# Optimization experiments

Measured on AMD Instinct MI355X. Metric: run time of the kernel, lower is better.

The kernel has to match this reference:

```python
import jax, jax.numpy as jnp
import numpy as np

NUM_FEATURES = 256   # 2**8
BOND_DIM = 16
N_CORES = 8          # log2(NUM_FEATURES)
BATCH = 262144


def _mpo_cores(mpo_weights, n, bond_dim):
    # Slice the flat parameter vector into n cores of shape (l, r, 2, 2).
    shapes = [(1, bond_dim, 2, 2)] + [(bond_dim, bond_dim, 2, 2)] * (n - 2) + [(bond_dim, 1, 2, 2)]
    cores, off = [], 0
    for s in shapes:
        sz = int(np.prod(s))
        cores.append(mpo_weights[off:off + sz].reshape(s))
        off += sz
    return cores


def _contract_mpo(cores):
    # Sequentially contract the tensor-train cores into the full (2^n, 2^n) matrix.
    # T has axes (bond, I, J) where I/J accumulate the row/col physical bits
    # in order i1..in / j1..jn, matching the original einsum + reshape.
    T = cores[0][0]          # (r, 2, 2)
    dim = 2
    for A in cores[1:]:      # A: (l, r2, 2, 2)
        T = jnp.einsum('aIJ,abkm->bIkJm', T, A).reshape(A.shape[1], dim * 2, dim * 2)
        dim *= 2
    return T[0]              # (2^n, 2^n)


def setup_inputs() -> dict:
    key = jax.random.key(0)
    k1, k2, k3 = jax.random.split(key, 3)
    total = 2 * 4 * BOND_DIM + (N_CORES - 2) * 4 * BOND_DIM ** 2  # 6272
    return {
        'x': jax.random.normal(k1, (BATCH, NUM_FEATURES), dtype=jnp.float32),
        'mpo_weights': jax.random.normal(k2, (total,), dtype=jnp.float32) * 0.1,
        'dense_kernel': jax.random.normal(k3, (NUM_FEATURES, 1), dtype=jnp.float32) * 0.1,
        'dense_bias': jnp.zeros((1,), dtype=jnp.float32),
    }


def reference(x, mpo_weights, dense_kernel, dense_bias):
    W = _contract_mpo(_mpo_cores(mpo_weights, N_CORES, BOND_DIM))  # (256, 256)
    h = jnp.square(x @ W)                                          # (B, 256)
    return h @ dense_kernel + dense_bias                           # (B, 1)
```

## Files before the change

kernel.cpp:

```cpp
#include <hip/hip_runtime.h>
#include <hip/hip_bf16.h>

typedef _Float16 half8 __attribute__((ext_vector_type(8)));
typedef float    floatx4 __attribute__((ext_vector_type(4)));

#define WSCALE      4096.0f
#define WSCALE_INV  (1.0f/(4096.0f*4096.0f))

#define WF16_OFF 8192

__global__ __launch_bounds__(256)
void mpo_prep(const float* __restrict__ w, _Float16* __restrict__ Wf) {
    __shared__ __align__(16) float wL[6272];
    __shared__ __align__(16) float sL[8704];
    __shared__ __align__(16) float tuL[8192];
    const int tid = threadIdx.x;

    {
        const floatx4* s4 = reinterpret_cast<const floatx4*>(w);
        floatx4* d4 = reinterpret_cast<floatx4*>(wL);
        for (int i = tid; i < 1568; i += 256) d4[i] = s4[i];
    }
    __syncthreads();

    {
        int li = tid;
        int mm = li & 3, kk = (li >> 2) & 3, c = li >> 4;
        int k1 = kk >> 1, k2 = kk & 1, m1 = mm >> 1, m2 = mm & 1;
        float s = 0.f;
#pragma unroll
        for (int b = 0; b < 16; ++b)
            s += wL[b * 4 + k1 * 2 + m1] * wL[64 + b * 64 + c * 4 + k2 * 2 + m2];
        sL[li] = s;
    }
    {
        const int i0 = (tid >> 4) * 4, j0 = (tid & 15) * 4;
        const float* Ab = wL + 1088 + (i0 >> 2) * 64;
        const float* Bb = wL + 2112 + j0;
        float acc[4][4] = {};
#pragma unroll
        for (int b = 0; b < 16; ++b) {
            floatx4 ar = *reinterpret_cast<const floatx4*>(Ab + b * 4);
            floatx4 br = *reinterpret_cast<const floatx4*>(Bb + b * 64);
#pragma unroll
            for (int r = 0; r < 4; ++r)
#pragma unroll
                for (int s = 0; s < 4; ++s) acc[r][s] += ar[r] * br[s];
        }
#pragma unroll
        for (int r = 0; r < 4; ++r)
#pragma unroll
        for (int s = 0; s < 4; ++s) {
            int i = i0 + r, j = j0 + s;
            sL[256 + (i >> 2) * 256 + (j >> 2) * 16 +
               ((i >> 1) & 1) * 8 + ((j >> 1) & 1) * 4 + (i & 1) * 2 + (j & 1)] = acc[r][s];
        }
    }
    {
        const int i0 = (tid >> 4) * 4, j0 = (tid & 15) * 4;
        const float* Ab = wL + 3136 + (i0 >> 2) * 64;
        const float* Bb = wL + 4160 + j0;
        float acc[4][4] = {};
#pragma unroll
        for (int b = 0; b < 16; ++b) {
            floatx4 ar = *reinterpret_cast<const floatx4*>(Ab + b * 4);
            floatx4 br = *reinterpret_cast<const floatx4*>(Bb + b * 64);
#pragma unroll
            for (int r = 0; r < 4; ++r)
#pragma unroll
                for (int s = 0; s < 4; ++s) acc[r][s] += ar[r] * br[s];
        }
#pragma unroll
        for (int r = 0; r < 4; ++r)
#pragma unroll
        for (int s = 0; s < 4; ++s) {
            int i = i0 + r, j = j0 + s;
            sL[4352 + (i >> 2) * 256 + (j >> 2) * 16 +
               ((i >> 1) & 1) * 8 + ((j >> 1) & 1) * 4 + (i & 1) * 2 + (j & 1)] = acc[r][s];
        }
    }
    {
        int li = tid;
        int mm = li & 3, kk = (li >> 2) & 3, a = li >> 4;
        int k1 = kk >> 1, k2 = kk & 1, m1 = mm >> 1, m2 = mm & 1;
        float s = 0.f;
#pragma unroll
        for (int b = 0; b < 16; ++b)
            s += wL[5184 + a * 64 + b * 4 + k1 * 2 + m1] * wL[6208 + b * 4 + k2 * 2 + m2];
        sL[8448 + li] = s;
    }
    __syncthreads();

    {
        const int p0 = (tid >> 6) * 4, q0 = (tid & 63) * 4;
        float acc[4][4] = {};
#pragma unroll
        for (int a = 0; a < 16; ++a) {
            floatx4 pr = *reinterpret_cast<const floatx4*>(sL + a * 16 + p0);
            floatx4 qr = *reinterpret_cast<const floatx4*>(sL + 256 + a * 256 + q0);
#pragma unroll
            for (int r = 0; r < 4; ++r)
#pragma unroll
                for (int s = 0; s < 4; ++s) acc[r][s] += pr[r] * qr[s];
        }
#pragma unroll
        for (int r = 0; r < 4; ++r)
#pragma unroll
        for (int s = 0; s < 4; ++s) {
            int p = p0 + r, q = q0 + s;
            tuL[(q >> 4) * 256 + ((p >> 2) * 4 + ((q >> 2) & 3)) * 16 +
                (p & 3) * 4 + (q & 3)] = acc[r][s];
        }
    }
    {
        const int r0 = (tid >> 2) * 4, q0 = (tid & 3) * 4;
        float acc[4][4] = {};
#pragma unroll
        for (int b = 0; b < 16; ++b) {
            floatx4 ar = *reinterpret_cast<const floatx4*>(sL + 4352 + (r0 >> 4) * 256 + b * 16 + (r0 & 15));
            floatx4 br = *reinterpret_cast<const floatx4*>(sL + 8448 + b * 16 + q0);
#pragma unroll
            for (int r = 0; r < 4; ++r)
#pragma unroll
                for (int s = 0; s < 4; ++s) acc[r][s] += ar[r] * br[s];
        }
#pragma unroll
        for (int r = 0; r < 4; ++r)
#pragma unroll
        for (int s = 0; s < 4; ++s)
            tuL[4096 + (r0 + r) * 16 + q0 + s] = acc[r][s];
    }
    __syncthreads();

    {
        int idx = blockIdx.x * 256 + tid;
        int J4 = idx & 255, I4 = idx >> 8;
        int I16 = I4 >> 4, kc = (I4 >> 2) & 3, k2v = I4 & 3;
        int mc = (J4 >> 2) & 3, m2v = J4 & 3;
        int J16 = J4 >> 4;
        const float* Uc = tuL + 4096 + (((kc * 4 + mc) * 4 + k2v) * 4 + m2v);
        float s = 0.f;
#pragma unroll
        for (int a = 0; a < 16; ++a)
            s += tuL[(a * 16 + I16) * 16 + J16] * Uc[a * 256];
        int nn = J4 >> 4, lr = J4 & 15, kq = I4 >> 5, gg = (I4 >> 3) & 3, jj = I4 & 7;
        Wf[(((nn * 8 + kq) * 64) + gg * 16 + lr) * 8 + jj] = (_Float16)(s * WSCALE);
    }
}

__global__ __launch_bounds__(512, 2)
void mpo_main(const float* __restrict__ x, const _Float16* __restrict__ Wf,
              const float* __restrict__ dk, const float* __restrict__ bias,
              float* __restrict__ out) {
    extern __shared__ _Float16 Wl[];
    float* dkL = reinterpret_cast<float*>(Wl + 65536);

    const int tid  = threadIdx.x;
    const int lane = tid & 63;
    const int wave = tid >> 6;
    const int lrow = lane & 15;
    const int g    = lane >> 4;

    const long blockbase = (long)blockIdx.x * 1024;
    const float* xb = x + (blockbase + wave * 16 + lrow) * 256 + g * 8;
    const int SET_STRIDE = 128 * 256;

    half8 a[8];
    floatx4 lo[8], hi[8];

#define SB()  __builtin_amdgcn_sched_barrier(0)
#define XLD(i, xn) do { const float* p_ = (xn) + (i) * 32;              \
                     lo[i] = *reinterpret_cast<const floatx4*>(p_);     \
                     hi[i] = *reinterpret_cast<const floatx4*>(p_ + 4); } while (0)
#define XLD_ALL(xn) do { XLD(0,xn); XLD(1,xn); XLD(2,xn); XLD(3,xn); \
                         XLD(4,xn); XLD(5,xn); XLD(6,xn); XLD(7,xn); } while (0)
#define XCVT(i) do { half8 f_;                                                \
                     f_[0] = (_Float16)lo[i][0]; f_[1] = (_Float16)lo[i][1];  \
                     f_[2] = (_Float16)lo[i][2]; f_[3] = (_Float16)lo[i][3];  \
                     f_[4] = (_Float16)hi[i][0]; f_[5] = (_Float16)hi[i][1];  \
                     f_[6] = (_Float16)hi[i][2]; f_[7] = (_Float16)hi[i][3];  \
                     a[i] = f_; } while (0)
#define XCVT_ALL() do { XCVT(0); XCVT(1); XCVT(2); XCVT(3); \
                        XCVT(4); XCVT(5); XCVT(6); XCVT(7); } while (0)

    XLD_ALL(xb);
    SB();
    {
        const floatx4* src = reinterpret_cast<const floatx4*>(Wf);
        floatx4* dst = reinterpret_cast<floatx4*>(Wl);
#pragma unroll
        for (int i = 0; i < 16; ++i)
            dst[tid + i * 512] = src[tid + i * 512];
    }
    if (tid < 256) dkL[tid] = dk[tid];
    const float bs = bias[0];
    __syncthreads();

    float kreg[16];
#pragma unroll
    for (int n = 0; n < 16; ++n) kreg[n] = dkL[n * 16 + lrow];

    XCVT_ALL();
    XLD_ALL(xb + SET_STRIDE);
    SB();

    const half8* Wv = reinterpret_cast<const half8*>(Wl);

#pragma unroll 1
    for (int s = 0; s < 8; ++s) {
        float rp[4] = {0, 0, 0, 0};
#pragma unroll 1
        for (int n = 0; n < 16; ++n) {
            const half8* Wn = Wv + n * 512 + lane;
            floatx4 c0 = {0, 0, 0, 0};
#pragma unroll
            for (int kk = 0; kk < 8; ++kk)
                c0 = __builtin_amdgcn_mfma_f32_16x16x32_f16(a[kk], Wn[kk * 64], c0, 0, 0, 0);
            const float kv = kreg[n];
#pragma unroll
            for (int r = 0; r < 4; ++r)
                rp[r] += c0[r] * c0[r] * kv;
        }

        if (s < 7) { XCVT_ALL(); }
        if (s < 6) { XLD_ALL(xb + (s + 2) * SET_STRIDE); }
        SB();

#pragma unroll
        for (int r = 0; r < 4; ++r) {
            float v = rp[r];
            v += __shfl_xor(v, 1);
            v += __shfl_xor(v, 2);
            v += __shfl_xor(v, 4);
            v += __shfl_xor(v, 8);
            rp[r] = v;
        }
        if (lrow == 0) {
            floatx4 o;
#pragma unroll
            for (int r = 0; r < 4; ++r) o[r] = rp[r] * WSCALE_INV + bs;
            *reinterpret_cast<floatx4*>(out + blockbase + s * 128 + wave * 16 + g * 4) = o;
        }
        SB();
    }
}

extern "C" void kernel_launch(void* const* d_in, const int* in_sizes, int n_in,
                              void* d_out, int out_size, void* d_ws, size_t ws_size,
                              hipStream_t stream) {
    const float* x    = (const float*)d_in[0];
    const float* w    = (const float*)d_in[1];
    const float* dk   = (const float*)d_in[2];
    const float* bias = (const float*)d_in[3];
    float* out = (float*)d_out;
    float* ws  = (float*)d_ws;

    _Float16* Wf16 = (_Float16*)(ws + WF16_OFF);

    static bool attr_set = false;
    if (!attr_set) {
        hipFuncSetAttribute((const void*)mpo_main,
                            hipFuncAttributeMaxDynamicSharedMemorySize, 132096);
        attr_set = true;
    }

    mpo_prep<<<256, 256, 0, stream>>>(w, Wf16);

    mpo_main<<<256, 512, 132096, stream>>>(x, Wf16, dk, bias, out);
}
```

Before: 62.60 us.

## Process two row tiles per wave to reuse each LDS weight fragment twice

Each wave now handles two 16-row tiles at once, so every W fragment loaded from LDS feeds two MFMAs and LDS read traffic per row is halved. The loop runs 4 passes of 256 rows instead of 8 of 128, with double x prefetch buffers (A and B sets). kreg is dropped in favour of reading dk from LDS inside the loop, which frees registers for the extra buffers. The cost is much higher VGPR pressure under launch_bounds(512,2), which may cause spills or lower occupancy, and fewer passes leave less room for the prefetch to overlap with compute.

Measured after the change: 92.11 us. 47.1% more time.

```diff
diff --git a/kernel.cpp b/kernel.cpp
--- a/kernel.cpp
+++ b/kernel.cpp
@@ -162,28 +162,32 @@
     const int g    = lane >> 4;
 
     const long blockbase = (long)blockIdx.x * 1024;
-    const float* xb = x + (blockbase + wave * 16 + lrow) * 256 + g * 8;
-    const int SET_STRIDE = 128 * 256;
-
-    half8 a[8];
-    floatx4 lo[8], hi[8];
+    const float* xb = x + (blockbase + wave * 32 + lrow) * 256 + g * 8;
+    const int PASS_STRIDE = 256 * 256;
+    const int SET_STRIDE  = 16 * 256;
+
+    half8 a0[8], a1[8];
+    floatx4 loA[8], hiA[8], loB[8], hiB[8];
 
 #define SB()  __builtin_amdgcn_sched_barrier(0)
-#define XLD(i, xn) do { const float* p_ = (xn) + (i) * 32;              \
-                     lo[i] = *reinterpret_cast<const floatx4*>(p_);     \
-                     hi[i] = *reinterpret_cast<const floatx4*>(p_ + 4); } while (0)
-#define XLD_ALL(xn) do { XLD(0,xn); XLD(1,xn); XLD(2,xn); XLD(3,xn); \
-                         XLD(4,xn); XLD(5,xn); XLD(6,xn); XLD(7,xn); } while (0)
-#define XCVT(i) do { half8 f_;                                                \
-                     f_[0] = (_Float16)lo[i][0]; f_[1] = (_Float16)lo[i][1];  \
-                     f_[2] = (_Float16)lo[i][2]; f_[3] = (_Float16)lo[i][3];  \
-                     f_[4] = (_Float16)hi[i][0]; f_[5] = (_Float16)hi[i][1];  \
-                     f_[6] = (_Float16)hi[i][2]; f_[7] = (_Float16)hi[i][3];  \
-                     a[i] = f_; } while (0)
-#define XCVT_ALL() do { XCVT(0); XCVT(1); XCVT(2); XCVT(3); \
-                        XCVT(4); XCVT(5); XCVT(6); XCVT(7); } while (0)
-
-    XLD_ALL(xb);
+#define XLD8(lo, hi, xn) do { _Pragma("unroll")                          \
+    for (int i_ = 0; i_ < 8; ++i_) {                                     \
+        const float* p_ = (xn) + i_ * 32;                                \
+        lo[i_] = *reinterpret_cast<const floatx4*>(p_);                  \
+        hi[i_] = *reinterpret_cast<const floatx4*>(p_ + 4);              \
+    } } while (0)
+#define XCVT8(a, lo, hi) do { _Pragma("unroll")                          \
+    for (int i_ = 0; i_ < 8; ++i_) {                                     \
+        half8 f_;                                                        \
+        f_[0] = (_Float16)lo[i_][0]; f_[1] = (_Float16)lo[i_][1];        \
+        f_[2] = (_Float16)lo[i_][2]; f_[3] = (_Float16)lo[i_][3];        \
+        f_[4] = (_Float16)hi[i_][0]; f_[5] = (_Float16)hi[i_][1];        \
+        f_[6] = (_Float16)hi[i_][2]; f_[7] = (_Float16)hi[i_][3];        \
+        a[i_] = f_;                                                      \
+    } } while (0)
+
+    XLD8(loA, hiA, xb);
+    XLD8(loB, hiB, xb + SET_STRIDE);
     SB();
     {
         const floatx4* src = reinterpret_cast<const floatx4*>(Wf);
@@ -196,50 +200,61 @@
     const float bs = bias[0];
     __syncthreads();
 
-    float kreg[16];
-#pragma unroll
-    for (int n = 0; n < 16; ++n) kreg[n] = dkL[n * 16 + lrow];
-
-    XCVT_ALL();
-    XLD_ALL(xb + SET_STRIDE);
+    XCVT8(a0, loA, hiA);
+    XLD8(loA, hiA, xb + PASS_STRIDE);
+    XCVT8(a1, loB, hiB);
+    XLD8(loB, hiB, xb + PASS_STRIDE + SET_STRIDE);
     SB();
 
     const half8* Wv = reinterpret_cast<const half8*>(Wl);
 
 #pragma unroll 1
-    for (int s = 0; s < 8; ++s) {
-        float rp[4] = {0, 0, 0, 0};
+    for (int p = 0; p < 4; ++p) {
+        float rp0[4] = {0, 0, 0, 0}, rp1[4] = {0, 0, 0, 0};
 #pragma unroll 1
         for (int n = 0; n < 16; ++n) {
+            const float kv = dkL[n * 16 + lrow];
             const half8* Wn = Wv + n * 512 + lane;
-            floatx4 c0 = {0, 0, 0, 0};
-#pragma unroll
-            for (int kk = 0; kk < 8; ++kk)
-                c0 = __builtin_amdgcn_mfma_f32_16x16x32_f16(a[kk], Wn[kk * 64], c0, 0, 0, 0);
-            const float kv = kreg[n];
-#pragma unroll
-            for (int r = 0; r < 4; ++r)
-                rp[r] += c0[r] * c0[r] * kv;
-        }
-
-        if (s < 7) { XCVT_ALL(); }
-        if (s < 6) { XLD_ALL(xb + (s + 2) * SET_STRIDE); }
-        SB();
+            floatx4 c0 = {0, 0, 0, 0}, c1 = {0, 0, 0, 0};
+#pragma unroll
+            for (int kk = 0; kk < 8; ++kk) {
+                half8 b = Wn[kk * 64];
+                c0 = __builtin_amdgcn_mfma_f32_16x16x32_f16(a0[kk], b, c0, 0, 0, 0);
+                c1 = __builtin_amdgcn_mfma_f32_16x16x32_f16(a1[kk], b, c1, 0, 0, 0);
+            }
+#pragma unroll
+            for (int r = 0; r < 4; ++r) {
+                rp0[r] += c0[r] * c0[r] * kv;
+                rp1[r] += c1[r] * c1[r] * kv;
+            }
+        }
 
 #pragma unroll
         for (int r = 0; r < 4; ++r) {
-            float v = rp[r];
-            v += __shfl_xor(v, 1);
-            v += __shfl_xor(v, 2);
-            v += __shfl_xor(v, 4);
-            v += __shfl_xor(v, 8);
-            rp[r] = v;
+            float v0 = rp0[r], v1 = rp1[r];
+            v0 += __shfl_xor(v0, 1); v1 += __shfl_xor(v1, 1);
+            v0 += __shfl_xor(v0, 2); v1 += __shfl_xor(v1, 2);
+            v0 += __shfl_xor(v0, 4); v1 += __shfl_xor(v1, 4);
+            v0 += __shfl_xor(v0, 8); v1 += __shfl_xor(v1, 8);
+            rp0[r] = v0; rp1[r] = v1;
         }
         if (lrow == 0) {
-            floatx4 o;
-#pragma unroll
-            for (int r = 0; r < 4; ++r) o[r] = rp[r] * WSCALE_INV + bs;
-            *reinterpret_cast<floatx4*>(out + blockbase + s * 128 + wave * 16 + g * 4) = o;
+            floatx4 o0, o1;
+#pragma unroll
+            for (int r = 0; r < 4; ++r) {
+                o0[r] = rp0[r] * WSCALE_INV + bs;
+                o1[r] = rp1[r] * WSCALE_INV + bs;
+            }
+            float* ob = out + blockbase + p * 256 + wave * 32 + g * 4;
+            *reinterpret_cast<floatx4*>(ob)      = o0;
+            *reinterpret_cast<floatx4*>(ob + 16) = o1;
+        }
+
+        if (p < 3) {
+            XCVT8(a0, loA, hiA);
+            if (p < 2) { XLD8(loA, hiA, xb + (p + 2) * PASS_STRIDE); }
+            XCVT8(a1, loB, hiB);
+            if (p < 2) { XLD8(loB, hiB, xb + (p + 2) * PASS_STRIDE + SET_STRIDE); }
         }
         SB();
     }
```

## Switch main GEMM to 32x32x16 MFMA tiles with half-split x pipelining

Applied to the files above, without the earlier changes.

Replaces the 16x16x32 MFMA tiling with 32x32x16 MFMA, so each wave processes 32 rows per step and the precomputed W is stored in a matching layout. x loads are split into two halves double-buffered across iterations, and the reduction and output stores are reworked for the 32-wide accumulator. This cuts LDS reads of W per FLOP and the number of MFMA issues, at the cost of more accumulator registers (16 floats for c and 16 for rp), which may lower occupancy or cause spills.

Measured after the change: 66.34 us. +6.0%, slower.

```diff
diff --git a/kernel.cpp b/kernel.cpp
--- a/kernel.cpp
+++ b/kernel.cpp
@@ -3,6 +3,7 @@
 
 typedef _Float16 half8 __attribute__((ext_vector_type(8)));
 typedef float    floatx4 __attribute__((ext_vector_type(4)));
+typedef float    floatx16 __attribute__((ext_vector_type(16)));
 
 #define WSCALE      4096.0f
 #define WSCALE_INV  (1.0f/(4096.0f*4096.0f))
@@ -143,8 +144,8 @@
 #pragma unroll
         for (int a = 0; a < 16; ++a)
             s += tuL[(a * 16 + I16) * 16 + J16] * Uc[a * 256];
-        int nn = J4 >> 4, lr = J4 & 15, kq = I4 >> 5, gg = (I4 >> 3) & 3, jj = I4 & 7;
-        Wf[(((nn * 8 + kq) * 64) + gg * 16 + lr) * 8 + jj] = (_Float16)(s * WSCALE);
+        int nn = J4 >> 5, cc = J4 & 31, kq = I4 >> 4, hh = (I4 >> 3) & 1, jj = I4 & 7;
+        Wf[(((nn * 16 + kq) * 64) + hh * 32 + cc) * 8 + jj] = (_Float16)(s * WSCALE);
     }
 }
 
@@ -158,32 +159,34 @@
     const int tid  = threadIdx.x;
     const int lane = tid & 63;
     const int wave = tid >> 6;
-    const int lrow = lane & 15;
-    const int g    = lane >> 4;
+    const int col  = lane & 31;
+    const int hi   = lane >> 5;
 
     const long blockbase = (long)blockIdx.x * 1024;
-    const float* xb = x + (blockbase + wave * 16 + lrow) * 256 + g * 8;
-    const int SET_STRIDE = 128 * 256;
-
-    half8 a[8];
-    floatx4 lo[8], hi[8];
+    const float* xr = x + (blockbase + wave * 32 + col) * 256 + hi * 8;
+    const int SS = 256 * 256;
+
+    half8 a[16];
+    floatx4 lob[8], hib[8];
 
 #define SB()  __builtin_amdgcn_sched_barrier(0)
-#define XLD(i, xn) do { const float* p_ = (xn) + (i) * 32;              \
-                     lo[i] = *reinterpret_cast<const floatx4*>(p_);     \
-                     hi[i] = *reinterpret_cast<const floatx4*>(p_ + 4); } while (0)
-#define XLD_ALL(xn) do { XLD(0,xn); XLD(1,xn); XLD(2,xn); XLD(3,xn); \
-                         XLD(4,xn); XLD(5,xn); XLD(6,xn); XLD(7,xn); } while (0)
-#define XCVT(i) do { half8 f_;                                                \
-                     f_[0] = (_Float16)lo[i][0]; f_[1] = (_Float16)lo[i][1];  \
-                     f_[2] = (_Float16)lo[i][2]; f_[3] = (_Float16)lo[i][3];  \
-                     f_[4] = (_Float16)hi[i][0]; f_[5] = (_Float16)hi[i][1];  \
-                     f_[6] = (_Float16)hi[i][2]; f_[7] = (_Float16)hi[i][3];  \
-                     a[i] = f_; } while (0)
-#define XCVT_ALL() do { XCVT(0); XCVT(1); XCVT(2); XCVT(3); \
-                        XCVT(4); XCVT(5); XCVT(6); XCVT(7); } while (0)
-
-    XLD_ALL(xb);
+#define XLDH(s, h) do { _Pragma("unroll")                                \
+    for (int i_ = 0; i_ < 8; ++i_) {                                     \
+        const float* p_ = xr + (s) * SS + ((h) * 8 + i_) * 16;           \
+        lob[i_] = *reinterpret_cast<const floatx4*>(p_);                 \
+        hib[i_] = *reinterpret_cast<const floatx4*>(p_ + 4);             \
+    } } while (0)
+#define XCVTH(h) do { _Pragma("unroll")                                  \
+    for (int i_ = 0; i_ < 8; ++i_) {                                     \
+        half8 f_;                                                        \
+        f_[0] = (_Float16)lob[i_][0]; f_[1] = (_Float16)lob[i_][1];      \
+        f_[2] = (_Float16)lob[i_][2]; f_[3] = (_Float16)lob[i_][3];      \
+        f_[4] = (_Float16)hib[i_][0]; f_[5] = (_Float16)hib[i_][1];      \
+        f_[6] = (_Float16)hib[i_][2]; f_[7] = (_Float16)hib[i_][3];      \
+        a[(h) * 8 + i_] = f_;                                            \
+    } } while (0)
+
+    XLDH(0, 0);
     SB();
     {
         const floatx4* src = reinterpret_cast<const floatx4*>(Wf);
@@ -196,51 +199,56 @@
     const float bs = bias[0];
     __syncthreads();
 
-    float kreg[16];
-#pragma unroll
-    for (int n = 0; n < 16; ++n) kreg[n] = dkL[n * 16 + lrow];
-
-    XCVT_ALL();
-    XLD_ALL(xb + SET_STRIDE);
+    float kreg[8];
+#pragma unroll
+    for (int n = 0; n < 8; ++n) kreg[n] = dkL[n * 32 + col];
+
+    XCVTH(0);
+    XLDH(0, 1);
     SB();
+    XCVTH(1);
+    XLDH(1, 0);
+    SB();
 
     const half8* Wv = reinterpret_cast<const half8*>(Wl);
 
 #pragma unroll 1
-    for (int s = 0; s < 8; ++s) {
-        float rp[4] = {0, 0, 0, 0};
+    for (int s = 0; s < 4; ++s) {
+        floatx16 rp = {0,0,0,0,0,0,0,0,0,0,0,0,0,0,0,0};
 #pragma unroll 1
-        for (int n = 0; n < 16; ++n) {
-            const half8* Wn = Wv + n * 512 + lane;
-            floatx4 c0 = {0, 0, 0, 0};
-#pragma unroll
-            for (int kk = 0; kk < 8; ++kk)
-                c0 = __builtin_amdgcn_mfma_f32_16x16x32_f16(a[kk], Wn[kk * 64], c0, 0, 0, 0);
+        for (int n = 0; n < 8; ++n) {
+            const half8* Wn = Wv + n * 1024 + lane;
+            floatx16 c = {0,0,0,0,0,0,0,0,0,0,0,0,0,0,0,0};
+#pragma unroll
+            for (int kk = 0; kk < 16; ++kk)
+                c = __builtin_amdgcn_mfma_f32_32x32x16_f16(a[kk], Wn[kk * 64], c, 0, 0, 0);
             const float kv = kreg[n];
 #pragma unroll
-            for (int r = 0; r < 4; ++r)
-                rp[r] += c0[r] * c0[r] * kv;
-        }
-
-        if (s < 7) { XCVT_ALL(); }
-        if (s < 6) { XLD_ALL(xb + (s + 2) * SET_STRIDE); }
+            for (int r = 0; r < 16; ++r) rp[r] += c[r] * c[r] * kv;
+        }
+
+        if (s < 3) { XCVTH(0); XLDH(s + 1, 1); }
         SB();
 
 #pragma unroll
-        for (int r = 0; r < 4; ++r) {
+        for (int r = 0; r < 16; ++r) {
             float v = rp[r];
             v += __shfl_xor(v, 1);
             v += __shfl_xor(v, 2);
             v += __shfl_xor(v, 4);
             v += __shfl_xor(v, 8);
+            v += __shfl_xor(v, 16);
             rp[r] = v;
         }
-        if (lrow == 0) {
-            floatx4 o;
-#pragma unroll
-            for (int r = 0; r < 4; ++r) o[r] = rp[r] * WSCALE_INV + bs;
-            *reinterpret_cast<floatx4*>(out + blockbase + s * 128 + wave * 16 + g * 4) = o;
-        }
+        if (col == 0) {
+            float* ob = out + blockbase + s * 256 + wave * 32 + hi * 4;
+#pragma unroll
+            for (int r = 0; r < 16; ++r)
+                ob[(r & 3) + 8 * (r >> 2)] = rp[r] * WSCALE_INV + bs;
+        }
+
+        if (s < 3) { XCVTH(1); }
+        if (s < 2) { XLDH(s + 2, 0); }
         SB();
     }
 }
```
